# Optimization experiments

Hardware: AMD Instinct MI355X
Metric: run time of the kernel (lower is better)

The kernel has to match this reference:

```python
import jax, jax.numpy as jnp
import numpy as np

OBS, ACT, H, O, B = 256, 64, 1024, 8, 4096
ALPHA, GAMMA, ACT_LIMIT = 0.2, 0.99, 1.0
LOG_STD_MIN, LOG_STD_MAX = -20.0, 2.0
D = OBS + ACT + O  # intra-Q input dim


def setup_inputs() -> dict:
    key = jax.random.key(0)
    ks = iter(jax.random.split(key, 64))
    w = lambda shape: (jax.random.normal(next(ks), shape) * 0.05).astype(jnp.float32)
    inp = {}
    inp["state"] = jax.random.normal(next(ks), (B, OBS), jnp.float32)
    inp["action"] = jnp.tanh(jax.random.normal(next(ks), (B, ACT), jnp.float32))
    inp["next_state"] = jax.random.normal(next(ks), (B, OBS), jnp.float32)
    inp["reward"] = jax.random.normal(next(ks), (B, 1), jnp.float32)
    inp["done"] = jnp.zeros((B, 1), jnp.float32)
    inp["noise"] = jax.random.normal(next(ks), (B, ACT), jnp.float32)
    inp["option"] = jax.random.randint(next(ks), (B,), 0, O, jnp.int32)
    # online inter-Q (q1,q2 stacked on leading axis): obs -> H -> H -> O
    inp["interq_W1"], inp["interq_b1"] = w((2, OBS, H)), w((2, H))
    inp["interq_W2"], inp["interq_b2"] = w((2, H, H)), w((2, H))
    inp["interq_W3"], inp["interq_b3"] = w((2, H, O)), w((2, O))
    # target inter-Q
    inp["tinterq_W1"], inp["tinterq_b1"] = w((2, OBS, H)), w((2, H))
    inp["tinterq_W2"], inp["tinterq_b2"] = w((2, H, H)), w((2, H))
    inp["tinterq_W3"], inp["tinterq_b3"] = w((2, H, O)), w((2, O))
    # intra-Q (q1,q2 stacked): [obs,act,onehot] -> H -> H -> 1
    inp["intraq_W1"], inp["intraq_b1"] = w((2, D, H)), w((2, H))
    inp["intraq_W2"], inp["intraq_b2"] = w((2, H, H)), w((2, H))
    inp["intraq_W3"], inp["intraq_b3"] = w((2, H, 1)), w((2, 1))
    # per-option squashed-Gaussian policies: obs -> H -> H -> (mu, log_std)
    inp["pol_W1"], inp["pol_b1"] = w((O, OBS, H)), w((O, H))
    inp["pol_W2"], inp["pol_b2"] = w((O, H, H)), w((O, H))
    inp["pol_Wmu"], inp["pol_bmu"] = w((O, H, ACT)), w((O, ACT))
    inp["pol_Wls"], inp["pol_bls"] = w((O, H, ACT)), w((O, ACT))
    # per-option termination (beta) nets: obs -> H -> 1, sigmoid
    inp["beta_W1"], inp["beta_b1"] = w((O, OBS, H)), w((O, H))
    inp["beta_W2"], inp["beta_b2"] = w((O, H, 1)), w((O, 1))
    return inp


def _mlp2_k(x, W1, b1, W2, b2, W3, b3):
    # x: [B,in], params stacked over leading k -> [k,B,out]
    h = jax.nn.relu(jnp.einsum('bi,kih->kbh', x, W1) + b1[:, None, :])
    h = jax.nn.relu(jnp.einsum('kbh,khg->kbg', h, W2) + b2[:, None, :])
    return jnp.einsum('kbg,kgo->kbo', h, W3) + b3[:, None, :]


def _forward(state, action, next_state, reward, done, noise,
             interq_W1, interq_b1, interq_W2, interq_b2, interq_W3, interq_b3,
             tinterq_W1, tinterq_b1, tinterq_W2, tinterq_b2, tinterq_W3, tinterq_b3,
             intraq_W1, intraq_b1, intraq_W2, intraq_b2, intraq_W3, intraq_b3,
             pol_W1, pol_b1, pol_W2, pol_b2, pol_Wmu, pol_bmu, pol_Wls, pol_bls,
             beta_W1, beta_b1, beta_W2, beta_b2, option):
    idx = jnp.arange(state.shape[0])
    onehot = jax.nn.one_hot(option, O, dtype=state.dtype)
    # intra Q on (state, action, onehot)
    xq = jnp.concatenate([state, action, onehot], axis=-1)  # [B,D]
    q_intra = _mlp2_k(xq, intraq_W1, intraq_b1, intraq_W2, intraq_b2, intraq_W3, intraq_b3)
    q1_intra, q2_intra = q_intra[0], q_intra[1]  # [B,1]
    # option-routed policy: compute all options, gather top-1 (grouped-MoE form)
    h = jax.nn.relu(jnp.einsum('bi,oih->boh', state, pol_W1) + pol_b1)      # [B,O,H]
    h = jax.nn.relu(jnp.einsum('boh,ohg->bog', h, pol_W2) + pol_b2)         # [B,O,H]
    mu = (jnp.einsum('bog,oga->boa', h, pol_Wmu) + pol_bmu)[idx, option]    # [B,ACT]
    ls = (jnp.einsum('bog,oga->boa', h, pol_Wls) + pol_bls)[idx, option]
    ls = jnp.clip(ls, LOG_STD_MIN, LOG_STD_MAX)
    pre = mu + jnp.exp(ls) * noise  # reparameterized pre-tanh action
    LOG2PI = jnp.float32(np.log(2.0 * np.pi))
    logp = jnp.sum(-0.5 * noise**2 - ls - 0.5 * LOG2PI, axis=-1)
    logp = logp - jnp.sum(2.0 * (jnp.log(jnp.float32(2.0)) - pre - jax.nn.softplus(-2.0 * pre)), axis=-1)  # [B]
    current_actions = ACT_LIMIT * jnp.tanh(pre)  # [B,ACT]
    # option-routed termination prob on next_state
    hb = jax.nn.relu(jnp.einsum('bi,oih->boh', next_state, beta_W1) + beta_b1)
    blog = jnp.einsum('boh,oh->bo', hb, beta_W2[..., 0]) + beta_b2[:, 0]
    beta_prob = jax.nn.sigmoid(blog)[idx, option][:, None]  # [B,1]
    # TD target (no-grad in torch)
    q_t = _mlp2_k(next_state, tinterq_W1, tinterq_b1, tinterq_W2, tinterq_b2, tinterq_W3, tinterq_b3)
    q_inter_targ = jnp.minimum(q_t[0], q_t[1])  # [B,O]
    q_cur = q_inter_targ[idx, option][:, None]
    q_on = _mlp2_k(next_state, interq_W1, interq_b1, interq_W2, interq_b2, interq_W3, interq_b3)
    next_opt = jnp.argmax(jnp.minimum(q_on[0], q_on[1]), axis=-1)  # greedy next option
    q_next = q_inter_targ[idx, next_opt][:, None]
    bp = jax.lax.stop_gradient(beta_prob)
    backup = jax.lax.stop_gradient(
        reward + GAMMA * (1.0 - done) * ((1.0 - bp) * q_cur + bp * q_next))
    loss_intra_q = jnp.mean((q1_intra - backup) ** 2) + jnp.mean((q2_intra - backup) ** 2)
    q_pi = jax.lax.stop_gradient(jnp.minimum(q1_intra, q2_intra))[:, 0]
    loss_intra_pi = jnp.mean(ALPHA * logp - q_pi)
    return (loss_intra_q, loss_intra_pi, current_actions, logp, beta_prob)


def reference(state, action, next_state, reward, done, noise,
              interq_W1, interq_b1, interq_W2, interq_b2, interq_W3, interq_b3,
              tinterq_W1, tinterq_b1, tinterq_W2, tinterq_b2, tinterq_W3, tinterq_b3,
              intraq_W1, intraq_b1, intraq_W2, intraq_b2, intraq_W3, intraq_b3,
              pol_W1, pol_b1, pol_W2, pol_b2, pol_Wmu, pol_bmu, pol_Wls, pol_bls,
              beta_W1, beta_b1, beta_W2, beta_b2, option):
    return _forward(state, action, next_state, reward, done, noise,
                    interq_W1, interq_b1, interq_W2, interq_b2, interq_W3, interq_b3,
                    tinterq_W1, tinterq_b1, tinterq_W2, tinterq_b2, tinterq_W3, tinterq_b3,
                    intraq_W1, intraq_b1, intraq_W2, intraq_b2, intraq_W3, intraq_b3,
                    pol_W1, pol_b1, pol_W2, pol_b2, pol_Wmu, pol_bmu, pol_Wls, pol_bls,
                    beta_W1, beta_b1, beta_W2, beta_b2, option)
```

## Files before the change

kernel.cpp:

```cpp
#include <hip/hip_runtime.h>
#include <stdint.h>

#define B_SZ 4096
#define OBS 256
#define ACT 64
#define HID 1024
#define NOPT 8

typedef __attribute__((ext_vector_type(8))) short short8;
typedef __attribute__((ext_vector_type(4))) float floatx4;
typedef __attribute__((ext_vector_type(4))) unsigned int u32x4;

constexpr long long OFF_WT_I1 = 0;
constexpr long long OFF_WT_I2 = OFF_WT_I1 + 2LL*1024*256*2;
constexpr long long OFF_WT_T1 = OFF_WT_I2 + 2LL*1024*1024*2;
constexpr long long OFF_WT_T2 = OFF_WT_T1 + 2LL*1024*256*2;
constexpr long long OFF_WT_X1 = OFF_WT_T2 + 2LL*1024*1024*2;
constexpr long long OFF_WT_X2 = OFF_WT_X1 + 2LL*1024*384*2;
constexpr long long OFF_WT_P1 = OFF_WT_X2 + 2LL*1024*1024*2;
constexpr long long OFF_WT_P2 = OFF_WT_P1 + 8LL*1024*256*2;
constexpr long long OFF_WT_ML = OFF_WT_P2 + 8LL*1024*1024*2;
constexpr long long OFF_WT_B1 = OFF_WT_ML + 8LL*128*1024*2;
constexpr long long OFF_XQ    = OFF_WT_B1 + 8LL*1024*256*2;
constexpr long long OFF_NS    = OFF_XQ + 4096LL*384*2;
constexpr long long OFF_AGS   = OFF_NS + 4096LL*256*2;
constexpr long long OFF_AGN   = OFF_AGS + 4224LL*256*2;
constexpr long long OFF_HAX   = OFF_AGN + 4224LL*256*2;
constexpr long long OFF_HAI   = OFF_HAX + 2LL*4096*1024*2;
constexpr long long OFF_HAT   = OFF_HAI + 2LL*4096*1024*2;
constexpr long long OFF_HAP   = OFF_HAT + 2LL*4096*1024*2;
constexpr long long OFF_HAB   = OFF_HAP + 4224LL*1024*2;
constexpr long long OFF_HBP   = OFF_HAB + 4224LL*1024*2;
constexpr long long OFF_QI    = OFF_HBP + 4224LL*1024*2;
constexpr long long OFF_QON   = OFF_QI + 2LL*8*4096*4;
constexpr long long OFF_QT    = OFF_QON + 2LL*8*4096*8*4;
constexpr long long OFF_MULS  = OFF_QT + 2LL*8*4096*8*4;
constexpr long long OFF_PERM  = OFF_MULS + 4224LL*128*4;
constexpr long long OFF_OPTG  = OFF_PERM + 4096LL*4;
constexpr long long OFF_BP    = OFF_OPTG + ((4224LL*4 + 255) & ~255LL);
constexpr long long OFF_LOGP  = OFF_BP + 4096LL*4;
constexpr long long OFF_TILEB = OFF_LOGP + 4096LL*4;
constexpr long long OFF_TILEC = OFF_TILEB + 272LL*64;
constexpr long long OFF_TILED = OFF_TILEC + 232LL*64;
constexpr long long WS_TOTAL  = OFF_TILED + 40LL*64;

struct Tile {
  long long aOff, wOff, cOff;
  int mStart, mEnd, K, nCols, flags, biasSel, biasOff, redSel, redOff, pad0;
};
struct Ptrs { const float* bias[9]; const float* w3[3]; };
struct TrSrcs { const float* p[11]; };

__device__ __forceinline__ unsigned short f2bf(float x){
  union { float f; unsigned u; } v; v.f = x;
  unsigned r = v.u + 0x7fffu + ((v.u >> 16) & 1u);
  return (unsigned short)(r >> 16);
}
__device__ __forceinline__ float bf2f(unsigned short h){
  union { float f; unsigned u; } v; v.u = ((unsigned)h) << 16; return v.f;
}

__device__ const long long tr_ws[11] = {256*1024,1024*1024,256*1024,1024*1024,328*1024,1024*1024,256*1024,1024*1024,1024*64,1024*64,256*1024};
__device__ const long long tr_ts[11] = {1024*256,1024*1024,1024*256,1024*1024,1024*384,1024*1024,1024*256,1024*1024,128*1024,128*1024,1024*256};
__device__ const long long tr_dst[11] = {OFF_WT_I1,OFF_WT_I2,OFF_WT_T1,OFF_WT_T2,OFF_WT_X1,OFF_WT_X2,OFF_WT_P1,OFF_WT_P2,OFF_WT_ML,OFF_WT_ML+64LL*1024*2,OFF_WT_B1};

__device__ const int t2_cum[12] = {0,128,640,768,1280,1472,1984,2496,4544,4672,4800,5312};
__device__ const int t2_nk[11]  = {4,16,4,16,6,16,4,16,16,16,4};
__device__ const int t2_N[11]   = {1024,1024,1024,1024,1024,1024,1024,1024,64,64,1024};
__device__ const int t2_K[11]   = {256,1024,256,1024,328,1024,256,1024,1024,1024,256};
__device__ const int t2_Kp[11]  = {256,1024,256,1024,384,1024,256,1024,1024,1024,256};

__global__ __launch_bounds__(256)
void k_tr(char* __restrict__ wsB, TrSrcs srcs){
  __shared__ float lds[64*68];
  int id = blockIdx.x, j = 0;
  while (id >= t2_cum[j+1]) j++;
  int t = id - t2_cum[j];
  int nk = t2_nk[j], nn = t2_N[j] >> 6;
  int per = nk*nn;
  int z = t / per, r = t % per;
  int kt = r % nk, nt = r / nk;
  int K = t2_K[j], Kp = t2_Kp[j], N = t2_N[j];
  const float* src = srcs.p[j] + (long long)z * tr_ws[j];
  unsigned short* dst = (unsigned short*)(wsB + tr_dst[j]) + (long long)z * tr_ts[j];
  int k0 = kt*64, n0 = nt*64;
  int tid = threadIdx.x;
  int kl = tid >> 2, nc = tid & 3;
  int krow = k0 + kl;
  const float* s = src + (long long)krow*N + n0 + nc*16;
  #pragma unroll
  for (int i=0;i<4;i++){
    float4 v = (krow < K) ? *(const float4*)(s + i*4) : make_float4(0.f,0.f,0.f,0.f);
    *(float4*)(&lds[kl*68 + nc*16 + i*4]) = v;
  }
  __syncthreads();
  int nl = tid >> 2, kc = tid & 3;
  unsigned int w[8];
  #pragma unroll
  for (int p=0;p<8;p++){
    float a = lds[(kc*16 + 2*p)*68 + nl];
    float b = lds[(kc*16 + 2*p + 1)*68 + nl];
    w[p] = (unsigned)f2bf(a) | ((unsigned)f2bf(b) << 16);
  }
  u32x4 o0 = {w[0],w[1],w[2],w[3]}, o1 = {w[4],w[5],w[6],w[7]};
  char* d = (char*)(dst + (long long)(n0+nl)*Kp + k0 + kc*16);
  *(u32x4*)d = o0; *(u32x4*)(d + 16) = o1;
}

__global__ void k_route(char* __restrict__ wsB, const int* __restrict__ option,
                        float* __restrict__ out){
  __shared__ int cnt[NOPT], off[NOPT+1], cur[NOPT], ctiles[NOPT], toff[NOPT+1];
  int tid = threadIdx.x;
  int* perm = (int*)(wsB + OFF_PERM);
  int* optg = (int*)(wsB + OFF_OPTG);
  Tile* tb = (Tile*)(wsB + OFF_TILEB);
  Tile* tc = (Tile*)(wsB + OFF_TILEC);
  Tile* tdt = (Tile*)(wsB + OFF_TILED);
  if (tid < NOPT) cnt[tid] = 0;
  __syncthreads();
  for (int b = tid; b < B_SZ; b += 256) atomicAdd(&cnt[option[b]], 1);
  __syncthreads();
  if (tid == 0){
    off[0] = 0; toff[0] = 0;
    for (int o=0;o<NOPT;o++){
      off[o+1] = off[o] + cnt[o];
      ctiles[o] = (cnt[o] + 127) >> 7;
      toff[o+1] = toff[o] + ctiles[o];
      cur[o] = off[o];
    }
    out[0] = 0.f; out[1] = 0.f;
  }
  __syncthreads();
  for (int b = tid; b < B_SZ; b += 256){
    int o = option[b];
    int pos = atomicAdd(&cur[o], 1);
    perm[pos] = b; optg[pos] = o;
  }
  __syncthreads();
  if (tid < 192){
    int task = tid/32, mt = tid%32, z = task&1, net = task>>1;
    int ms = mt*128;
    Tile T{};
    T.mStart = ms; T.mEnd = 4096; T.nCols = 1024; T.flags = 0;
    T.redSel = 0; T.redOff = 0;
    if (net==0){ T.K=384; T.aOff = OFF_XQ + (long long)ms*768; T.wOff = OFF_WT_X1 + (long long)z*786432; T.cOff = OFF_HAX + (long long)z*8388608; T.biasSel=0; }
    else if (net==1){ T.K=256; T.aOff = OFF_NS + (long long)ms*512; T.wOff = OFF_WT_I1 + (long long)z*524288; T.cOff = OFF_HAI + (long long)z*8388608; T.biasSel=1; }
    else { T.K=256; T.aOff = OFF_NS + (long long)ms*512; T.wOff = OFF_WT_T1 + (long long)z*524288; T.cOff = OFF_HAT + (long long)z*8388608; T.biasSel=2; }
    T.biasOff = z*1024;
    tb[tid] = T;
    Tile C{};
    C.mStart = ms; C.mEnd = 4096; C.K = 1024; C.nCols = 1024;
    if (net==0){ C.flags=2; C.aOff = OFF_HAX + (long long)z*8388608 + (long long)ms*2048; C.wOff = OFF_WT_X2 + (long long)z*2097152; C.cOff = OFF_QI + (long long)z*131072; C.biasSel=5; C.redSel=0; C.redOff=z*1024; }
    else if (net==1){ C.flags=3; C.aOff = OFF_HAI + (long long)z*8388608 + (long long)ms*2048; C.wOff = OFF_WT_I2 + (long long)z*2097152; C.cOff = OFF_QON + (long long)z*1048576; C.biasSel=6; C.redSel=1; C.redOff=z*8192; }
    else { C.flags=3; C.aOff = OFF_HAT + (long long)z*8388608 + (long long)ms*2048; C.wOff = OFF_WT_T2 + (long long)z*2097152; C.cOff = OFF_QT + (long long)z*1048576; C.biasSel=7; C.redSel=2; C.redOff=z*8192; }
    C.biasOff = z*1024;
    tc[tid] = C;
  }
  if (tid < NOPT){
    int o = tid, base = toff[o], gs = off[o], ge = off[o+1];
    for (int t=0; t<ctiles[o]; t++){
      int ms = gs + t*128;
      Tile P{};
      P.mStart=ms; P.mEnd=ge; P.K=256; P.nCols=1024; P.flags=0;
      P.aOff = OFF_AGS + (long long)ms*512; P.wOff = OFF_WT_P1 + (long long)o*524288;
      P.cOff = OFF_HAP; P.biasSel=3; P.biasOff=o*1024;
      tb[192 + base + t] = P;
      Tile Bt{};
      Bt.mStart=ms; Bt.mEnd=ge; Bt.K=256; Bt.nCols=1024; Bt.flags=0;
      Bt.aOff = OFF_AGN + (long long)ms*512; Bt.wOff = OFF_WT_B1 + (long long)o*524288;
      Bt.cOff = OFF_HAB; Bt.biasSel=4; Bt.biasOff=o*1024;
      tb[232 + base + t] = Bt;
      Tile C2{};
      C2.mStart=ms; C2.mEnd=ge; C2.K=1024; C2.nCols=1024; C2.flags=0;
      C2.aOff = OFF_HAP + (long long)ms*2048; C2.wOff = OFF_WT_P2 + (long long)o*2097152;
      C2.cOff = OFF_HBP; C2.biasSel=8; C2.biasOff=o*1024;
      tc[192 + base + t] = C2;
      Tile M{};
      M.mStart=ms; M.mEnd=ge; M.K=1024; M.nCols=128; M.flags=1;
      M.aOff = OFF_HBP + (long long)ms*2048; M.wOff = OFF_WT_ML + (long long)o*262144;
      M.cOff = OFF_MULS; M.biasSel=-1;
      tdt[base + t] = M;
    }
  }
  __syncthreads();
  int tT = toff[NOPT];
  for (int s = tT + tid; s < 40; s += 256){
    tb[192+s].K = 0; tb[232+s].K = 0; tc[192+s].K = 0; tdt[s].K = 0;
  }
}

__global__ void k_prep(char* __restrict__ wsB, const float* __restrict__ state,
                       const float* __restrict__ action, const float* __restrict__ nstate,
                       const int* __restrict__ option){
  int blk = blockIdx.x, tid = threadIdx.x;
  const int* perm = (const int*)(wsB + OFF_PERM);
  if (blk < 4224){
    unsigned short* agS = (unsigned short*)(wsB + OFF_AGS);
    unsigned short* agN = (unsigned short*)(wsB + OFF_AGN);
    long long o = (long long)blk*256 + tid;
    if (blk < 4096){
      long long src = (long long)perm[blk]*256 + tid;
      agS[o] = f2bf(state[src]); agN[o] = f2bf(nstate[src]);
    } else { agS[o] = 0; agN[o] = 0; }
  } else if (blk < 8320){
    int b = blk - 4224;
    unsigned short* xq = (unsigned short*)(wsB + OFF_XQ);
    for (int c = tid; c < 384; c += 256){
      float v;
      if (c < 256) v = state[(long long)b*256 + c];
      else if (c < 320) v = action[(long long)b*64 + (c-256)];
      else if (c < 328) v = (option[b] == (c-320)) ? 1.f : 0.f;
      else v = 0.f;
      xq[(long long)b*384 + c] = f2bf(v);
    }
  } else {
    long long i = (long long)(blk-8320)*1024 + tid;
    unsigned short* nsb = (unsigned short*)(wsB + OFF_NS);
    #pragma unroll
    for (int k=0;k<4;k++){ nsb[i] = f2bf(nstate[i]); i += 256; }
  }
}

__global__ __launch_bounds__(256, 2)
void k_gemm(char* __restrict__ wsB, long long tileOff, Ptrs ptrs){
  __shared__ unsigned short As[128*64];
  __shared__ unsigned short Bs[256*64];
  int nx = gridDim.x, T = gridDim.y;
  int id = blockIdx.y*nx + blockIdx.x;
  int xb, yt;
  if ((T & 7) == 0){
    int xcd = id & 7, g = id >> 3;
    xb = g % nx; yt = (g / nx) * 8 + xcd;
  } else { xb = blockIdx.x; yt = blockIdx.y; }
  Tile t = ((const Tile*)(wsB + tileOff))[yt];
  if (t.K == 0) return;
  int n0 = xb * 256;
  if (n0 >= t.nCols) return;

  int tid = threadIdx.x;
  int wave = tid >> 6, lane = tid & 63;
  int wm = wave & 1, wn = wave >> 1;
  int quad = lane >> 4, l16 = lane & 15;

  const floatx4 fzero = {0.f,0.f,0.f,0.f};
  floatx4 acc[4][8];
  #pragma unroll
  for (int mi=0;mi<4;mi++)
    #pragma unroll
    for (int ni=0;ni<8;ni++) acc[mi][ni] = fzero;

  long long rowBytes = (long long)t.K*2;
  const char* Abase = wsB + t.aOff;
  const char* Bbase = wsB + t.wOff + (long long)n0*rowBytes;

  int ra0 = tid >> 2, ka0 = (tid & 3) * 16;
  int ra1 = ra0 + 64;
  const char* gA0 = Abase + (long long)ra0*rowBytes + ka0;
  const char* gA1 = Abase + (long long)ra1*rowBytes + ka0;
  const char* gBp[4];
  #pragma unroll
  for (int j=0;j<4;j++){
    int rb = (tid >> 2) + j*64;
    gBp[j] = Bbase + (long long)rb*rowBytes + ka0;
  }

  u32x4 pA[4], pB[8];
  #define PREFETCH(KBB) { \
    long long _kb = (KBB); \
    pA[0] = *(const u32x4*)(gA0 + _kb);      pA[1] = *(const u32x4*)(gA0 + _kb + 64); \
    pA[2] = *(const u32x4*)(gA1 + _kb);      pA[3] = *(const u32x4*)(gA1 + _kb + 64); \
    _Pragma("unroll") \
    for (int j=0;j<4;j++){ \
      pB[2*j]   = *(const u32x4*)(gBp[j] + _kb); \
      pB[2*j+1] = *(const u32x4*)(gBp[j] + _kb + 64); \
    } }
  #define STAGE() { \
    *(u32x4*)((char*)As + tid*16)         = pA[0]; \
    *(u32x4*)((char*)As + 8192 + tid*16)  = pA[1]; \
    *(u32x4*)((char*)As + 4096 + tid*16)  = pA[2]; \
    *(u32x4*)((char*)As + 12288 + tid*16) = pA[3]; \
    _Pragma("unroll") \
    for (int j=0;j<4;j++){ \
      *(u32x4*)((char*)Bs + j*4096 + tid*16)         = pB[2*j]; \
      *(u32x4*)((char*)Bs + 16384 + j*4096 + tid*16) = pB[2*j+1]; \
    } }

  int nkb = t.K >> 6;
  PREFETCH(0);
  STAGE();
  __syncthreads();
  for (int kb = 0; kb < nkb; kb++){
    if (kb + 1 < nkb) PREFETCH((long long)(kb+1)*128);
    #pragma unroll
    for (int h=0; h<2; h++){
      short8 af[4], bfr[8];
      #pragma unroll
      for (int mi=0;mi<4;mi++)
        af[mi] = *(const short8*)((const char*)As + h*8192 + (wm*64 + mi*16 + l16)*64 + quad*16);
      #pragma unroll
      for (int ni=0;ni<8;ni++)
        bfr[ni] = *(const short8*)((const char*)Bs + h*16384 + (wn*128 + ni*16 + l16)*64 + quad*16);
      #pragma unroll
      for (int mi=0;mi<4;mi++)
        #pragma unroll
        for (int ni=0;ni<8;ni++)
          acc[mi][ni] = __builtin_amdgcn_mfma_f32_16x16x32_bf16(af[mi], bfr[ni], acc[mi][ni], 0, 0, 0);
    }
    __syncthreads();
    if (kb + 1 < nkb){
      STAGE();
      __syncthreads();
    }
  }
  #undef PREFETCH
  #undef STAGE

  if (t.flags <= 1){
    const float* bz = (t.biasSel >= 0) ? (ptrs.bias[t.biasSel] + t.biasOff) : nullptr;
    #pragma unroll
    for (int ni=0;ni<8;ni++){
      int col = n0 + wn*128 + ni*16 + l16;
      if (col >= t.nCols) continue;
      float bval = bz ? bz[col] : 0.f;
      #pragma unroll
      for (int mi=0;mi<4;mi++){
        int rbase = t.mStart + wm*64 + mi*16 + quad*4;
        floatx4 v = acc[mi][ni];
        #pragma unroll
        for (int r=0;r<4;r++){
          int grow = rbase + r;
          if (grow < t.mEnd){
            float x = v[r] + bval;
            if (t.flags == 0){
              x = fmaxf(x, 0.f);
              ((unsigned short*)(wsB + t.cOff))[(long long)grow*t.nCols + col] = f2bf(x);
            } else {
              ((float*)(wsB + t.cOff))[(long long)grow*t.nCols + col] = x;
            }
          }
        }
      }
    }
  } else {
    int NC = (t.flags == 2) ? 1 : 8;
    const float* w3 = ptrs.w3[t.redSel] + t.redOff;
    const float* bz = ptrs.bias[t.biasSel] + t.biasOff;
    int sl = xb*2 + wn;
    float* red = (float*)(wsB + t.cOff) + (long long)sl*4096*NC;
    float bv[8]; int colv[8];
    #pragma unroll
    for (int ni=0;ni<8;ni++){ colv[ni] = n0 + wn*128 + ni*16 + l16; bv[ni] = bz[colv[ni]]; }
    #pragma unroll
    for (int mi=0;mi<4;mi++){
      #pragma unroll
      for (int r=0;r<4;r++){
        int row = t.mStart + wm*64 + mi*16 + quad*4 + r;
        float v[8];
        #pragma unroll
        for (int c=0;c<8;c++) v[c] = 0.f;
        #pragma unroll
        for (int ni=0;ni<8;ni++){
          float x = fmaxf(acc[mi][ni][r] + bv[ni], 0.f);
          if (NC == 1) v[0] += x * w3[colv[ni]];
          else {
            #pragma unroll
            for (int c=0;c<8;c++) v[c] += x * w3[colv[ni]*8 + c];
          }
        }
        for (int c=0;c<NC;c++){
          float s = v[c];
          s += __shfl_xor(s,1); s += __shfl_xor(s,2); s += __shfl_xor(s,4); s += __shfl_xor(s,8);
          if (l16 == 0 && row < t.mEnd) red[(long long)row*NC + c] = s;
        }
      }
    }
  }
}

__global__ void k_bp(char* __restrict__ wsB, const float* __restrict__ noise,
                     const float* __restrict__ bmu, const float* __restrict__ bls,
                     const float* __restrict__ beW2, const float* __restrict__ beb2,
                     float* __restrict__ out){
  int job = blockIdx.x*4 + (threadIdx.x >> 6);
  int lane = threadIdx.x & 63;
  const int* perm = (const int*)(wsB + OFF_PERM);
  const int* optg = (const int*)(wsB + OFF_OPTG);
  if (job < B_SZ){
    int i = job, o = optg[i], b = perm[i];
    const float* muls = (const float*)(wsB + OFF_MULS);
    float* logp = (float*)(wsB + OFF_LOGP);
    float mu = muls[(long long)i*128 + lane] + bmu[o*ACT + lane];
    float ls = muls[(long long)i*128 + 64 + lane] + bls[o*ACT + lane];
    ls = fminf(fmaxf(ls, -20.f), 2.f);
    float nv = noise[(long long)b*ACT + lane];
    float pre = mu + expf(ls)*nv;
    out[2 + (long long)b*ACT + lane] = tanhf(pre);
    float xx = -2.f*pre;
    float sp = fmaxf(xx, 0.f) + log1pf(expf(-fabsf(xx)));
    const float LOG2PI = 1.8378770664093453f;
    const float LN2 = 0.6931471805599453f;
    float lp = -0.5f*nv*nv - ls - 0.5f*LOG2PI - 2.f*(LN2 - pre - sp);
    for (int s=32;s;s>>=1) lp += __shfl_xor(lp, s);
    if (lane == 0){ out[2 + (long long)B_SZ*ACT + b] = lp; logp[b] = lp; }
  } else {
    int i = job - B_SZ, o = optg[i], b = perm[i];
    const char* hrow = wsB + OFF_HAB + (long long)i*2048;
    const float* w = beW2 + (long long)o*HID;
    float* bp = (float*)(wsB + OFF_BP);
    short8 v0 = *(const short8*)(hrow + lane*16);
    short8 v1 = *(const short8*)(hrow + 1024 + lane*16);
    float acc = 0.f;
    #pragma unroll
    for (int e=0;e<8;e++){
      acc += bf2f((unsigned short)v0[e]) * w[lane*8 + e];
      acc += bf2f((unsigned short)v1[e]) * w[512 + lane*8 + e];
    }
    for (int s=32;s;s>>=1) acc += __shfl_xor(acc, s);
    if (lane == 0){
      float v = 1.f/(1.f + expf(-(acc + beb2[o])));
      out[2 + (long long)B_SZ*ACT + B_SZ + b] = v; bp[b] = v;
    }
  }
}

__global__ void k_td(const char* __restrict__ wsB, const int* __restrict__ option,
                     const float* __restrict__ reward, const float* __restrict__ done,
                     const float* __restrict__ xb3, const float* __restrict__ ib3,
                     const float* __restrict__ tb3, float* __restrict__ out){
  int b = blockIdx.x*256 + threadIdx.x;
  const float* qiP  = (const float*)(wsB + OFF_QI);
  const float* qonP = (const float*)(wsB + OFF_QON);
  const float* qtP  = (const float*)(wsB + OFF_QT);
  const float* bp   = (const float*)(wsB + OFF_BP);
  const float* logp = (const float*)(wsB + OFF_LOGP);
  float q1 = xb3[0], q2 = xb3[1];
  #pragma unroll
  for (int sl=0; sl<8; sl++){
    q1 += qiP[sl*4096 + b];
    q2 += qiP[32768 + sl*4096 + b];
  }
  float qons[2][8], qts[2][8];
  #pragma unroll
  for (int z=0;z<2;z++)
    #pragma unroll
    for (int o=0;o<8;o++){ qons[z][o] = ib3[z*8+o]; qts[z][o] = tb3[z*8+o]; }
  for (int z=0;z<2;z++){
    for (int sl=0; sl<8; sl++){
      long long base = ((long long)(z*8 + sl)*4096 + b)*8;
      #pragma unroll
      for (int o=0;o<8;o++){ qons[z][o] += qonP[base+o]; qts[z][o] += qtP[base+o]; }
    }
  }
  float qitv[NOPT];
  #pragma unroll
  for (int o=0;o<NOPT;o++) qitv[o] = fminf(qts[0][o], qts[1][o]);
  float qcur = qitv[option[b]];
  float best = -1e30f; int bo = 0;
  #pragma unroll
  for (int o=0;o<NOPT;o++){
    float v = fminf(qons[0][o], qons[1][o]);
    if (v > best){ best = v; bo = o; }
  }
  float qnext = qitv[bo];
  float bpv = bp[b];
  float backup = reward[b] + 0.99f*(1.f - done[b])*((1.f - bpv)*qcur + bpv*qnext);
  float d1 = q1 - backup, d2 = q2 - backup;
  float tq = d1*d1 + d2*d2;
  float qpi = fminf(q1, q2);
  float tp = 0.2f*logp[b] - qpi;
  for (int s=32;s;s>>=1){ tq += __shfl_xor(tq, s); tp += __shfl_xor(tp, s); }
  __shared__ float sq[4], sp2[4];
  int wave = threadIdx.x>>6, lane = threadIdx.x&63;
  if (lane==0){ sq[wave]=tq; sp2[wave]=tp; }
  __syncthreads();
  if (threadIdx.x==0){
    atomicAdd(&out[0], (sq[0]+sq[1]+sq[2]+sq[3])/(float)B_SZ);
    atomicAdd(&out[1], (sp2[0]+sp2[1]+sp2[2]+sp2[3])/(float)B_SZ);
  }
}

extern "C" void kernel_launch(void* const* d_in, const int* in_sizes, int n_in,
                              void* d_out, int out_size, void* d_ws, size_t ws_size,
                              hipStream_t stream){
  const float* state  = (const float*)d_in[0];
  const float* action = (const float*)d_in[1];
  const float* nstate = (const float*)d_in[2];
  const float* reward = (const float*)d_in[3];
  const float* done   = (const float*)d_in[4];
  const float* noise  = (const float*)d_in[5];
  const int*   option = (const int*)d_in[6];
  const float* iq_W1 = (const float*)d_in[7];  const float* iq_b1 = (const float*)d_in[8];
  const float* iq_W2 = (const float*)d_in[9];  const float* iq_b2 = (const float*)d_in[10];
  const float* iq_W3 = (const float*)d_in[11]; const float* iq_b3 = (const float*)d_in[12];
  const float* tq_W1 = (const float*)d_in[13]; const float* tq_b1 = (const float*)d_in[14];
  const float* tq_W2 = (const float*)d_in[15]; const float* tq_b2 = (const float*)d_in[16];
  const float* tq_W3 = (const float*)d_in[17]; const float* tq_b3 = (const float*)d_in[18];
  const float* xw_W1 = (const float*)d_in[19]; const float* xw_b1 = (const float*)d_in[20];
  const float* xw_W2 = (const float*)d_in[21]; const float* xw_b2 = (const float*)d_in[22];
  const float* xw_W3 = (const float*)d_in[23]; const float* xw_b3 = (const float*)d_in[24];
  const float* p_W1 = (const float*)d_in[25];  const float* p_b1 = (const float*)d_in[26];
  const float* p_W2 = (const float*)d_in[27];  const float* p_b2 = (const float*)d_in[28];
  const float* p_Wmu = (const float*)d_in[29]; const float* p_bmu = (const float*)d_in[30];
  const float* p_Wls = (const float*)d_in[31]; const float* p_bls = (const float*)d_in[32];
  const float* be_W1 = (const float*)d_in[33]; const float* be_b1 = (const float*)d_in[34];
  const float* be_W2 = (const float*)d_in[35]; const float* be_b2 = (const float*)d_in[36];
  float* out = (float*)d_out;
  char* wsB = (char*)d_ws;
  if ((long long)ws_size < WS_TOTAL) return;

  TrSrcs trs;
  trs.p[0]=iq_W1; trs.p[1]=iq_W2; trs.p[2]=tq_W1; trs.p[3]=tq_W2; trs.p[4]=xw_W1;
  trs.p[5]=xw_W2; trs.p[6]=p_W1; trs.p[7]=p_W2; trs.p[8]=p_Wmu; trs.p[9]=p_Wls; trs.p[10]=be_W1;
  Ptrs ptrs;
  ptrs.bias[0]=xw_b1; ptrs.bias[1]=iq_b1; ptrs.bias[2]=tq_b1; ptrs.bias[3]=p_b1; ptrs.bias[4]=be_b1;
  ptrs.bias[5]=xw_b2; ptrs.bias[6]=iq_b2; ptrs.bias[7]=tq_b2; ptrs.bias[8]=p_b2;
  ptrs.w3[0]=xw_W3; ptrs.w3[1]=iq_W3; ptrs.w3[2]=tq_W3;

  k_route<<<1, 256, 0, stream>>>(wsB, option, out);
  k_tr<<<5312, 256, 0, stream>>>(wsB, trs);
  k_prep<<<9344, 256, 0, stream>>>(wsB, state, action, nstate, option);
  k_gemm<<<dim3(4,272), 256, 0, stream>>>(wsB, OFF_TILEB, ptrs);
  k_gemm<<<dim3(4,232), 256, 0, stream>>>(wsB, OFF_TILEC, ptrs);
  k_gemm<<<dim3(1,40), 256, 0, stream>>>(wsB, OFF_TILED, ptrs);
  k_bp<<<2048, 256, 0, stream>>>(wsB, noise, p_bmu, p_bls, be_W2, be_b2, out);
  k_td<<<B_SZ/256, 256, 0, stream>>>(wsB, option, reward, done, xw_b3, iq_b3, tq_b3, out);
}
```

Before: 485.2 us.

## Drop LDS staging in GEMM for direct register loads; split-K the mu/logstd GEMM

The GEMM kernel no longer stages A and B tiles through shared memory. Each wave now loads its MFMA fragments straight from global memory into registers, double-buffered with no barriers. Separately, the small mu/log_std GEMM is split four ways along K into separate partial buffers, which k_bp sums, so the launch grows from 40 to 160 blocks. The aim is to remove LDS traffic and syncs and to raise parallelism in the tail GEMM. In exchange, blocks no longer share tile data, so global and L2 traffic rises and the 16-byte row-strided loads become uncoalesced.

Result: slower. 907.3 us (+87.0%).

```diff
diff --git a/kernel.cpp b/kernel.cpp
--- a/kernel.cpp
+++ b/kernel.cpp
@@ -35,18 +35,19 @@
 constexpr long long OFF_QON   = OFF_QI + 2LL*8*4096*4;
 constexpr long long OFF_QT    = OFF_QON + 2LL*8*4096*8*4;
 constexpr long long OFF_MULS  = OFF_QT + 2LL*8*4096*8*4;
-constexpr long long OFF_PERM  = OFF_MULS + 4224LL*128*4;
+constexpr long long MULS_CH   = 4224LL*128*4;
+constexpr long long OFF_PERM  = OFF_MULS + 4LL*MULS_CH;
 constexpr long long OFF_OPTG  = OFF_PERM + 4096LL*4;
 constexpr long long OFF_BP    = OFF_OPTG + ((4224LL*4 + 255) & ~255LL);
 constexpr long long OFF_LOGP  = OFF_BP + 4096LL*4;
 constexpr long long OFF_TILEB = OFF_LOGP + 4096LL*4;
 constexpr long long OFF_TILEC = OFF_TILEB + 272LL*64;
 constexpr long long OFF_TILED = OFF_TILEC + 232LL*64;
-constexpr long long WS_TOTAL  = OFF_TILED + 40LL*64;
+constexpr long long WS_TOTAL  = OFF_TILED + 160LL*64;
 
 struct Tile {
   long long aOff, wOff, cOff;
-  int mStart, mEnd, K, nCols, flags, biasSel, biasOff, redSel, redOff, pad0;
+  int mStart, mEnd, K, nCols, flags, biasSel, biasOff, redSel, redOff, kLen;
 };
 struct Ptrs { const float* bias[9]; const float* w3[3]; };
 struct TrSrcs { const float* p[11]; };
@@ -146,10 +147,10 @@
     if (net==0){ T.K=384; T.aOff = OFF_XQ + (long long)ms*768; T.wOff = OFF_WT_X1 + (long long)z*786432; T.cOff = OFF_HAX + (long long)z*8388608; T.biasSel=0; }
     else if (net==1){ T.K=256; T.aOff = OFF_NS + (long long)ms*512; T.wOff = OFF_WT_I1 + (long long)z*524288; T.cOff = OFF_HAI + (long long)z*8388608; T.biasSel=1; }
     else { T.K=256; T.aOff = OFF_NS + (long long)ms*512; T.wOff = OFF_WT_T1 + (long long)z*524288; T.cOff = OFF_HAT + (long long)z*8388608; T.biasSel=2; }
-    T.biasOff = z*1024;
+    T.biasOff = z*1024; T.kLen = T.K;
     tb[tid] = T;
     Tile C{};
-    C.mStart = ms; C.mEnd = 4096; C.K = 1024; C.nCols = 1024;
+    C.mStart = ms; C.mEnd = 4096; C.K = 1024; C.nCols = 1024; C.kLen = 1024;
     if (net==0){ C.flags=2; C.aOff = OFF_HAX + (long long)z*8388608 + (long long)ms*2048; C.wOff = OFF_WT_X2 + (long long)z*2097152; C.cOff = OFF_QI + (long long)z*131072; C.biasSel=5; C.redSel=0; C.redOff=z*1024; }
     else if (net==1){ C.flags=3; C.aOff = OFF_HAI + (long long)z*8388608 + (long long)ms*2048; C.wOff = OFF_WT_I2 + (long long)z*2097152; C.cOff = OFF_QON + (long long)z*1048576; C.biasSel=6; C.redSel=1; C.redOff=z*8192; }
     else { C.flags=3; C.aOff = OFF_HAT + (long long)z*8388608 + (long long)ms*2048; C.wOff = OFF_WT_T2 + (long long)z*2097152; C.cOff = OFF_QT + (long long)z*1048576; C.biasSel=7; C.redSel=2; C.redOff=z*8192; }
@@ -161,31 +162,37 @@
     for (int t=0; t<ctiles[o]; t++){
       int ms = gs + t*128;
       Tile P{};
-      P.mStart=ms; P.mEnd=ge; P.K=256; P.nCols=1024; P.flags=0;
+      P.mStart=ms; P.mEnd=ge; P.K=256; P.nCols=1024; P.flags=0; P.kLen=256;
       P.aOff = OFF_AGS + (long long)ms*512; P.wOff = OFF_WT_P1 + (long long)o*524288;
       P.cOff = OFF_HAP; P.biasSel=3; P.biasOff=o*1024;
       tb[192 + base + t] = P;
       Tile Bt{};
-      Bt.mStart=ms; Bt.mEnd=ge; Bt.K=256; Bt.nCols=1024; Bt.flags=0;
+      Bt.mStart=ms; Bt.mEnd=ge; Bt.K=256; Bt.nCols=1024; Bt.flags=0; Bt.kLen=256;
       Bt.aOff = OFF_AGN + (long long)ms*512; Bt.wOff = OFF_WT_B1 + (long long)o*524288;
       Bt.cOff = OFF_HAB; Bt.biasSel=4; Bt.biasOff=o*1024;
       tb[232 + base + t] = Bt;
       Tile C2{};
-      C2.mStart=ms; C2.mEnd=ge; C2.K=1024; C2.nCols=1024; C2.flags=0;
+      C2.mStart=ms; C2.mEnd=ge; C2.K=1024; C2.nCols=1024; C2.flags=0; C2.kLen=1024;
       C2.aOff = OFF_HAP + (long long)ms*2048; C2.wOff = OFF_WT_P2 + (long long)o*2097152;
       C2.cOff = OFF_HBP; C2.biasSel=8; C2.biasOff=o*1024;
       tc[192 + base + t] = C2;
-      Tile M{};
-      M.mStart=ms; M.mEnd=ge; M.K=1024; M.nCols=128; M.flags=1;
-      M.aOff = OFF_HBP + (long long)ms*2048; M.wOff = OFF_WT_ML + (long long)o*262144;
-      M.cOff = OFF_MULS; M.biasSel=-1;
-      tdt[base + t] = M;
+      #pragma unroll
+      for (int c=0;c<4;c++){
+        Tile M{};
+        M.mStart=ms; M.mEnd=ge; M.K=1024; M.nCols=128; M.flags=1; M.kLen=256;
+        M.aOff = OFF_HBP + (long long)ms*2048 + c*512;
+        M.wOff = OFF_WT_ML + (long long)o*262144 + c*512;
+        M.cOff = OFF_MULS + (long long)c*MULS_CH;
+        M.biasSel=-1;
+        tdt[c*40 + base + t] = M;
+      }
     }
   }
   __syncthreads();
   int tT = toff[NOPT];
   for (int s = tT + tid; s < 40; s += 256){
-    tb[192+s].K = 0; tb[232+s].K = 0; tc[192+s].K = 0; tdt[s].K = 0;
+    tb[192+s].kLen = 0; tb[232+s].kLen = 0; tc[192+s].kLen = 0;
+    tdt[s].kLen = 0; tdt[40+s].kLen = 0; tdt[80+s].kLen = 0; tdt[120+s].kLen = 0;
   }
 }
 
@@ -223,8 +230,6 @@
 
 __global__ __launch_bounds__(256, 2)
 void k_gemm(char* __restrict__ wsB, long long tileOff, Ptrs ptrs){
-  __shared__ unsigned short As[128*64];
-  __shared__ unsigned short Bs[256*64];
   int nx = gridDim.x, T = gridDim.y;
   int id = blockIdx.y*nx + blockIdx.x;
   int xb, yt;
@@ -233,7 +238,7 @@
     xb = g % nx; yt = (g / nx) * 8 + xcd;
   } else { xb = blockIdx.x; yt = blockIdx.y; }
   Tile t = ((const Tile*)(wsB + tileOff))[yt];
-  if (t.K == 0) return;
+  if (t.kLen == 0) return;
   int n0 = xb * 256;
   if (n0 >= t.nCols) return;
 
@@ -241,6 +246,7 @@
   int wave = tid >> 6, lane = tid & 63;
   int wm = wave & 1, wn = wave >> 1;
   int quad = lane >> 4, l16 = lane & 15;
+  int n0w = n0 + wn*128;
 
   const floatx4 fzero = {0.f,0.f,0.f,0.f};
   floatx4 acc[4][8];
@@ -249,77 +255,44 @@
     #pragma unroll
     for (int ni=0;ni<8;ni++) acc[mi][ni] = fzero;
 
-  long long rowBytes = (long long)t.K*2;
-  const char* Abase = wsB + t.aOff;
-  const char* Bbase = wsB + t.wOff + (long long)n0*rowBytes;
-
-  int ra0 = tid >> 2, ka0 = (tid & 3) * 16;
-  int ra1 = ra0 + 64;
-  const char* gA0 = Abase + (long long)ra0*rowBytes + ka0;
-  const char* gA1 = Abase + (long long)ra1*rowBytes + ka0;
-  const char* gBp[4];
-  #pragma unroll
-  for (int j=0;j<4;j++){
-    int rb = (tid >> 2) + j*64;
-    gBp[j] = Bbase + (long long)rb*rowBytes + ka0;
-  }
-
-  u32x4 pA[4], pB[8];
-  #define PREFETCH(KBB) { \
-    long long _kb = (KBB); \
-    pA[0] = *(const u32x4*)(gA0 + _kb);      pA[1] = *(const u32x4*)(gA0 + _kb + 64); \
-    pA[2] = *(const u32x4*)(gA1 + _kb);      pA[3] = *(const u32x4*)(gA1 + _kb + 64); \
-    _Pragma("unroll") \
-    for (int j=0;j<4;j++){ \
-      pB[2*j]   = *(const u32x4*)(gBp[j] + _kb); \
-      pB[2*j+1] = *(const u32x4*)(gBp[j] + _kb + 64); \
-    } }
-  #define STAGE() { \
-    *(u32x4*)((char*)As + tid*16)         = pA[0]; \
-    *(u32x4*)((char*)As + 8192 + tid*16)  = pA[1]; \
-    *(u32x4*)((char*)As + 4096 + tid*16)  = pA[2]; \
-    *(u32x4*)((char*)As + 12288 + tid*16) = pA[3]; \
-    _Pragma("unroll") \
-    for (int j=0;j<4;j++){ \
-      *(u32x4*)((char*)Bs + j*4096 + tid*16)         = pB[2*j]; \
-      *(u32x4*)((char*)Bs + 16384 + j*4096 + tid*16) = pB[2*j+1]; \
-    } }
-
-  int nkb = t.K >> 6;
-  PREFETCH(0);
-  STAGE();
-  __syncthreads();
-  for (int kb = 0; kb < nkb; kb++){
-    if (kb + 1 < nkb) PREFETCH((long long)(kb+1)*128);
-    #pragma unroll
-    for (int h=0; h<2; h++){
-      short8 af[4], bfr[8];
-      #pragma unroll
-      for (int mi=0;mi<4;mi++)
-        af[mi] = *(const short8*)((const char*)As + h*8192 + (wm*64 + mi*16 + l16)*64 + quad*16);
-      #pragma unroll
-      for (int ni=0;ni<8;ni++)
-        bfr[ni] = *(const short8*)((const char*)Bs + h*16384 + (wn*128 + ni*16 + l16)*64 + quad*16);
-      #pragma unroll
-      for (int mi=0;mi<4;mi++)
-        #pragma unroll
-        for (int ni=0;ni<8;ni++)
-          acc[mi][ni] = __builtin_amdgcn_mfma_f32_16x16x32_bf16(af[mi], bfr[ni], acc[mi][ni], 0, 0, 0);
-    }
-    __syncthreads();
-    if (kb + 1 < nkb){
-      STAGE();
-      __syncthreads();
-    }
-  }
-  #undef PREFETCH
-  #undef STAGE
+  long long rowB = (long long)t.K*2;
+  const char* Ab = wsB + t.aOff;
+  const char* Bb = wsB + t.wOff;
+  const char* pa[4]; const char* pb[8];
+  #pragma unroll
+  for (int mi=0;mi<4;mi++)
+    pa[mi] = Ab + (long long)(wm*64 + mi*16 + l16)*rowB + quad*16;
+  #pragma unroll
+  for (int ni=0;ni<8;ni++)
+    pb[ni] = Bb + (long long)(n0w + ni*16 + l16)*rowB + quad*16;
+
+  #define LD(dA, dB, KO) { \
+    _Pragma("unroll") for (int mi=0;mi<4;mi++) dA[mi] = *(const short8*)(pa[mi] + (KO)); \
+    _Pragma("unroll") for (int ni=0;ni<8;ni++) dB[ni] = *(const short8*)(pb[ni] + (KO)); }
+  #define MM(sA, sB) { \
+    _Pragma("unroll") for (int mi=0;mi<4;mi++) \
+      _Pragma("unroll") for (int ni=0;ni<8;ni++) \
+        acc[mi][ni] = __builtin_amdgcn_mfma_f32_16x16x32_bf16(sA[mi], sB[ni], acc[mi][ni], 0, 0, 0); }
+
+  int nkb = t.kLen >> 5;
+  short8 aC[4], bC[8], aN[4], bN[8];
+  LD(aC, bC, 0);
+  LD(aN, bN, 64);
+  for (int kb = 0; kb < nkb; kb += 2){
+    long long ko = (long long)kb*64;
+    MM(aC, bC);
+    if (kb + 2 < nkb) LD(aC, bC, ko + 128);
+    MM(aN, bN);
+    if (kb + 3 < nkb) LD(aN, bN, ko + 192);
+  }
+  #undef LD
+  #undef MM
 
   if (t.flags <= 1){
     const float* bz = (t.biasSel >= 0) ? (ptrs.bias[t.biasSel] + t.biasOff) : nullptr;
     #pragma unroll
     for (int ni=0;ni<8;ni++){
-      int col = n0 + wn*128 + ni*16 + l16;
+      int col = n0w + ni*16 + l16;
       if (col >= t.nCols) continue;
       float bval = bz ? bz[col] : 0.f;
       #pragma unroll
@@ -349,7 +322,7 @@
     float* red = (float*)(wsB + t.cOff) + (long long)sl*4096*NC;
     float bv[8]; int colv[8];
     #pragma unroll
-    for (int ni=0;ni<8;ni++){ colv[ni] = n0 + wn*128 + ni*16 + l16; bv[ni] = bz[colv[ni]]; }
+    for (int ni=0;ni<8;ni++){ colv[ni] = n0w + ni*16 + l16; bv[ni] = bz[colv[ni]]; }
     #pragma unroll
     for (int mi=0;mi<4;mi++){
       #pragma unroll
@@ -389,8 +362,13 @@
     int i = job, o = optg[i], b = perm[i];
     const float* muls = (const float*)(wsB + OFF_MULS);
     float* logp = (float*)(wsB + OFF_LOGP);
-    float mu = muls[(long long)i*128 + lane] + bmu[o*ACT + lane];
-    float ls = muls[(long long)i*128 + 64 + lane] + bls[o*ACT + lane];
+    float mu = bmu[o*ACT + lane];
+    float ls = bls[o*ACT + lane];
+    #pragma unroll
+    for (int c=0;c<4;c++){
+      mu += muls[(long long)c*(MULS_CH/4) + (long long)i*128 + lane];
+      ls += muls[(long long)c*(MULS_CH/4) + (long long)i*128 + 64 + lane];
+    }
     ls = fminf(fmaxf(ls, -20.f), 2.f);
     float nv = noise[(long long)b*ACT + lane];
     float pre = mu + expf(ls)*nv;
@@ -521,7 +499,7 @@
   k_prep<<<9344, 256, 0, stream>>>(wsB, state, action, nstate, option);
   k_gemm<<<dim3(4,272), 256, 0, stream>>>(wsB, OFF_TILEB, ptrs);
   k_gemm<<<dim3(4,232), 256, 0, stream>>>(wsB, OFF_TILEC, ptrs);
-  k_gemm<<<dim3(1,40), 256, 0, stream>>>(wsB, OFF_TILED, ptrs);
+  k_gemm<<<dim3(1,160), 256, 0, stream>>>(wsB, OFF_TILED, ptrs);
   k_bp<<<2048, 256, 0, stream>>>(wsB, noise, p_bmu, p_bls, be_W2, be_b2, out);
   k_td<<<B_SZ/256, 256, 0, stream>>>(wsB, option, reward, done, xw_b3, iq_b3, tq_b3, out);
 }
```

## Split policy head GEMM along K into four chunks, merge transpose into prep

Applied to the files above, without the earlier changes.

The mu/log-std head GEMM (K=1024, only 128 columns, 40 tiles) is split into four K-chunks of 256. Each chunk writes its own partial buffer, and k_bp sums the four partials, so the launch has 160 blocks instead of 40 and keeps more of the GPU busy. The weight-transpose kernel is folded into k_prep as extra blocks, which removes one launch and lets the two jobs overlap. The gemm kernel is also split into three identically compiled kernels. In exchange, the head needs more workspace and k_bp does extra partial-sum reads.

Measured after the change: 468.1 us. 1.04x faster.

```diff
diff --git a/kernel.cpp b/kernel.cpp
--- a/kernel.cpp
+++ b/kernel.cpp
@@ -35,18 +35,19 @@
 constexpr long long OFF_QON   = OFF_QI + 2LL*8*4096*4;
 constexpr long long OFF_QT    = OFF_QON + 2LL*8*4096*8*4;
 constexpr long long OFF_MULS  = OFF_QT + 2LL*8*4096*8*4;
-constexpr long long OFF_PERM  = OFF_MULS + 4224LL*128*4;
+constexpr long long MULS_CH   = 4224LL*128*4;
+constexpr long long OFF_PERM  = OFF_MULS + 4LL*MULS_CH;
 constexpr long long OFF_OPTG  = OFF_PERM + 4096LL*4;
 constexpr long long OFF_BP    = OFF_OPTG + ((4224LL*4 + 255) & ~255LL);
 constexpr long long OFF_LOGP  = OFF_BP + 4096LL*4;
 constexpr long long OFF_TILEB = OFF_LOGP + 4096LL*4;
 constexpr long long OFF_TILEC = OFF_TILEB + 272LL*64;
 constexpr long long OFF_TILED = OFF_TILEC + 232LL*64;
-constexpr long long WS_TOTAL  = OFF_TILED + 40LL*64;
+constexpr long long WS_TOTAL  = OFF_TILED + 160LL*64;
 
 struct Tile {
   long long aOff, wOff, cOff;
-  int mStart, mEnd, K, nCols, flags, biasSel, biasOff, redSel, redOff, pad0;
+  int mStart, mEnd, K, nCols, flags, biasSel, biasOff, redSel, redOff, kLen;
 };
 struct Ptrs { const float* bias[9]; const float* w3[3]; };
 struct TrSrcs { const float* p[11]; };
@@ -63,49 +64,11 @@
 __device__ const long long tr_ws[11] = {256*1024,1024*1024,256*1024,1024*1024,328*1024,1024*1024,256*1024,1024*1024,1024*64,1024*64,256*1024};
 __device__ const long long tr_ts[11] = {1024*256,1024*1024,1024*256,1024*1024,1024*384,1024*1024,1024*256,1024*1024,128*1024,128*1024,1024*256};
 __device__ const long long tr_dst[11] = {OFF_WT_I1,OFF_WT_I2,OFF_WT_T1,OFF_WT_T2,OFF_WT_X1,OFF_WT_X2,OFF_WT_P1,OFF_WT_P2,OFF_WT_ML,OFF_WT_ML+64LL*1024*2,OFF_WT_B1};
-
 __device__ const int t2_cum[12] = {0,128,640,768,1280,1472,1984,2496,4544,4672,4800,5312};
 __device__ const int t2_nk[11]  = {4,16,4,16,6,16,4,16,16,16,4};
 __device__ const int t2_N[11]   = {1024,1024,1024,1024,1024,1024,1024,1024,64,64,1024};
 __device__ const int t2_K[11]   = {256,1024,256,1024,328,1024,256,1024,1024,1024,256};
 __device__ const int t2_Kp[11]  = {256,1024,256,1024,384,1024,256,1024,1024,1024,256};
-
-__global__ __launch_bounds__(256)
-void k_tr(char* __restrict__ wsB, TrSrcs srcs){
-  __shared__ float lds[64*68];
-  int id = blockIdx.x, j = 0;
-  while (id >= t2_cum[j+1]) j++;
-  int t = id - t2_cum[j];
-  int nk = t2_nk[j], nn = t2_N[j] >> 6;
-  int per = nk*nn;
-  int z = t / per, r = t % per;
-  int kt = r % nk, nt = r / nk;
-  int K = t2_K[j], Kp = t2_Kp[j], N = t2_N[j];
-  const float* src = srcs.p[j] + (long long)z * tr_ws[j];
-  unsigned short* dst = (unsigned short*)(wsB + tr_dst[j]) + (long long)z * tr_ts[j];
-  int k0 = kt*64, n0 = nt*64;
-  int tid = threadIdx.x;
-  int kl = tid >> 2, nc = tid & 3;
-  int krow = k0 + kl;
-  const float* s = src + (long long)krow*N + n0 + nc*16;
-  #pragma unroll
-  for (int i=0;i<4;i++){
-    float4 v = (krow < K) ? *(const float4*)(s + i*4) : make_float4(0.f,0.f,0.f,0.f);
-    *(float4*)(&lds[kl*68 + nc*16 + i*4]) = v;
-  }
-  __syncthreads();
-  int nl = tid >> 2, kc = tid & 3;
-  unsigned int w[8];
-  #pragma unroll
-  for (int p=0;p<8;p++){
-    float a = lds[(kc*16 + 2*p)*68 + nl];
-    float b = lds[(kc*16 + 2*p + 1)*68 + nl];
-    w[p] = (unsigned)f2bf(a) | ((unsigned)f2bf(b) << 16);
-  }
-  u32x4 o0 = {w[0],w[1],w[2],w[3]}, o1 = {w[4],w[5],w[6],w[7]};
-  char* d = (char*)(dst + (long long)(n0+nl)*Kp + k0 + kc*16);
-  *(u32x4*)d = o0; *(u32x4*)(d + 16) = o1;
-}
 
 __global__ void k_route(char* __restrict__ wsB, const int* __restrict__ option,
                         float* __restrict__ out){
@@ -146,10 +109,10 @@
     if (net==0){ T.K=384; T.aOff = OFF_XQ + (long long)ms*768; T.wOff = OFF_WT_X1 + (long long)z*786432; T.cOff = OFF_HAX + (long long)z*8388608; T.biasSel=0; }
     else if (net==1){ T.K=256; T.aOff = OFF_NS + (long long)ms*512; T.wOff = OFF_WT_I1 + (long long)z*524288; T.cOff = OFF_HAI + (long long)z*8388608; T.biasSel=1; }
     else { T.K=256; T.aOff = OFF_NS + (long long)ms*512; T.wOff = OFF_WT_T1 + (long long)z*524288; T.cOff = OFF_HAT + (long long)z*8388608; T.biasSel=2; }
-    T.biasOff = z*1024;
+    T.biasOff = z*1024; T.kLen = T.K;
     tb[tid] = T;
     Tile C{};
-    C.mStart = ms; C.mEnd = 4096; C.K = 1024; C.nCols = 1024;
+    C.mStart = ms; C.mEnd = 4096; C.K = 1024; C.nCols = 1024; C.kLen = 1024;
     if (net==0){ C.flags=2; C.aOff = OFF_HAX + (long long)z*8388608 + (long long)ms*2048; C.wOff = OFF_WT_X2 + (long long)z*2097152; C.cOff = OFF_QI + (long long)z*131072; C.biasSel=5; C.redSel=0; C.redOff=z*1024; }
     else if (net==1){ C.flags=3; C.aOff = OFF_HAI + (long long)z*8388608 + (long long)ms*2048; C.wOff = OFF_WT_I2 + (long long)z*2097152; C.cOff = OFF_QON + (long long)z*1048576; C.biasSel=6; C.redSel=1; C.redOff=z*8192; }
     else { C.flags=3; C.aOff = OFF_HAT + (long long)z*8388608 + (long long)ms*2048; C.wOff = OFF_WT_T2 + (long long)z*2097152; C.cOff = OFF_QT + (long long)z*1048576; C.biasSel=7; C.redSel=2; C.redOff=z*8192; }
@@ -161,38 +124,81 @@
     for (int t=0; t<ctiles[o]; t++){
       int ms = gs + t*128;
       Tile P{};
-      P.mStart=ms; P.mEnd=ge; P.K=256; P.nCols=1024; P.flags=0;
+      P.mStart=ms; P.mEnd=ge; P.K=256; P.nCols=1024; P.flags=0; P.kLen=256;
       P.aOff = OFF_AGS + (long long)ms*512; P.wOff = OFF_WT_P1 + (long long)o*524288;
       P.cOff = OFF_HAP; P.biasSel=3; P.biasOff=o*1024;
       tb[192 + base + t] = P;
       Tile Bt{};
-      Bt.mStart=ms; Bt.mEnd=ge; Bt.K=256; Bt.nCols=1024; Bt.flags=0;
+      Bt.mStart=ms; Bt.mEnd=ge; Bt.K=256; Bt.nCols=1024; Bt.flags=0; Bt.kLen=256;
       Bt.aOff = OFF_AGN + (long long)ms*512; Bt.wOff = OFF_WT_B1 + (long long)o*524288;
       Bt.cOff = OFF_HAB; Bt.biasSel=4; Bt.biasOff=o*1024;
       tb[232 + base + t] = Bt;
       Tile C2{};
-      C2.mStart=ms; C2.mEnd=ge; C2.K=1024; C2.nCols=1024; C2.flags=0;
+      C2.mStart=ms; C2.mEnd=ge; C2.K=1024; C2.nCols=1024; C2.flags=0; C2.kLen=1024;
       C2.aOff = OFF_HAP + (long long)ms*2048; C2.wOff = OFF_WT_P2 + (long long)o*2097152;
       C2.cOff = OFF_HBP; C2.biasSel=8; C2.biasOff=o*1024;
       tc[192 + base + t] = C2;
-      Tile M{};
-      M.mStart=ms; M.mEnd=ge; M.K=1024; M.nCols=128; M.flags=1;
-      M.aOff = OFF_HBP + (long long)ms*2048; M.wOff = OFF_WT_ML + (long long)o*262144;
-      M.cOff = OFF_MULS; M.biasSel=-1;
-      tdt[base + t] = M;
+      #pragma unroll
+      for (int c=0;c<4;c++){
+        Tile M{};
+        M.mStart=ms; M.mEnd=ge; M.K=1024; M.nCols=128; M.flags=1; M.kLen=256;
+        M.aOff = OFF_HBP + (long long)ms*2048 + c*512;
+        M.wOff = OFF_WT_ML + (long long)o*262144 + c*512;
+        M.cOff = OFF_MULS + (long long)c*MULS_CH;
+        M.biasSel=-1;
+        tdt[c*40 + base + t] = M;
+      }
     }
   }
   __syncthreads();
   int tT = toff[NOPT];
   for (int s = tT + tid; s < 40; s += 256){
-    tb[192+s].K = 0; tb[232+s].K = 0; tc[192+s].K = 0; tdt[s].K = 0;
-  }
-}
-
-__global__ void k_prep(char* __restrict__ wsB, const float* __restrict__ state,
-                       const float* __restrict__ action, const float* __restrict__ nstate,
-                       const int* __restrict__ option){
-  int blk = blockIdx.x, tid = threadIdx.x;
+    tb[192+s].kLen = 0; tb[232+s].kLen = 0; tc[192+s].kLen = 0;
+    tdt[s].kLen = 0; tdt[40+s].kLen = 0; tdt[80+s].kLen = 0; tdt[120+s].kLen = 0;
+  }
+}
+
+__global__ __launch_bounds__(256)
+void k_prep(char* __restrict__ wsB, TrSrcs srcs, const float* __restrict__ state,
+            const float* __restrict__ action, const float* __restrict__ nstate,
+            const int* __restrict__ option){
+  __shared__ float lds[64*68];
+  int blk0 = blockIdx.x, tid = threadIdx.x;
+  if (blk0 < 5312){
+    int id = blk0, j = 0;
+    while (id >= t2_cum[j+1]) j++;
+    int t = id - t2_cum[j];
+    int nk = t2_nk[j], nn = t2_N[j] >> 6;
+    int per = nk*nn;
+    int z = t / per, r = t % per;
+    int kt = r % nk, nt = r / nk;
+    int K = t2_K[j], Kp = t2_Kp[j], N = t2_N[j];
+    const float* src = srcs.p[j] + (long long)z * tr_ws[j];
+    unsigned short* dst = (unsigned short*)(wsB + tr_dst[j]) + (long long)z * tr_ts[j];
+    int k0 = kt*64, n0 = nt*64;
+    int kl = tid >> 2, nc = tid & 3;
+    int krow = k0 + kl;
+    const float* s = src + (long long)krow*N + n0 + nc*16;
+    #pragma unroll
+    for (int i=0;i<4;i++){
+      float4 v = (krow < K) ? *(const float4*)(s + i*4) : make_float4(0.f,0.f,0.f,0.f);
+      *(float4*)(&lds[kl*68 + nc*16 + i*4]) = v;
+    }
+    __syncthreads();
+    int nl = tid >> 2, kc = tid & 3;
+    unsigned int w[8];
+    #pragma unroll
+    for (int p=0;p<8;p++){
+      float a = lds[(kc*16 + 2*p)*68 + nl];
+      float b = lds[(kc*16 + 2*p + 1)*68 + nl];
+      w[p] = (unsigned)f2bf(a) | ((unsigned)f2bf(b) << 16);
+    }
+    u32x4 o0 = {w[0],w[1],w[2],w[3]}, o1 = {w[4],w[5],w[6],w[7]};
+    char* d = (char*)(dst + (long long)(n0+nl)*Kp + k0 + kc*16);
+    *(u32x4*)d = o0; *(u32x4*)(d + 16) = o1;
+    return;
+  }
+  int blk = blk0 - 5312;
   const int* perm = (const int*)(wsB + OFF_PERM);
   if (blk < 4224){
     unsigned short* agS = (unsigned short*)(wsB + OFF_AGS);
@@ -221,8 +227,7 @@
   }
 }
 
-__global__ __launch_bounds__(256, 2)
-void k_gemm(char* __restrict__ wsB, long long tileOff, Ptrs ptrs){
+__device__ __forceinline__ void gemm_body(char* __restrict__ wsB, long long tileOff, const Ptrs& ptrs){
   __shared__ unsigned short As[128*64];
   __shared__ unsigned short Bs[256*64];
   int nx = gridDim.x, T = gridDim.y;
@@ -233,7 +238,7 @@
     xb = g % nx; yt = (g / nx) * 8 + xcd;
   } else { xb = blockIdx.x; yt = blockIdx.y; }
   Tile t = ((const Tile*)(wsB + tileOff))[yt];
-  if (t.K == 0) return;
+  if (t.kLen == 0) return;
   int n0 = xb * 256;
   if (n0 >= t.nCols) return;
 
@@ -285,7 +290,7 @@
       *(u32x4*)((char*)Bs + 16384 + j*4096 + tid*16) = pB[2*j+1]; \
     } }
 
-  int nkb = t.K >> 6;
+  int nkb = t.kLen >> 6;
   PREFETCH(0);
   STAGE();
   __syncthreads();
@@ -377,6 +382,13 @@
   }
 }
 
+__global__ __launch_bounds__(256, 2)
+void k_gemm_l1(char* __restrict__ wsB, long long tileOff, Ptrs ptrs){ gemm_body(wsB, tileOff, ptrs); }
+__global__ __launch_bounds__(256, 2)
+void k_gemm_l2(char* __restrict__ wsB, long long tileOff, Ptrs ptrs){ gemm_body(wsB, tileOff, ptrs); }
+__global__ __launch_bounds__(256, 2)
+void k_gemm_hd(char* __restrict__ wsB, long long tileOff, Ptrs ptrs){ gemm_body(wsB, tileOff, ptrs); }
+
 __global__ void k_bp(char* __restrict__ wsB, const float* __restrict__ noise,
                      const float* __restrict__ bmu, const float* __restrict__ bls,
                      const float* __restrict__ beW2, const float* __restrict__ beb2,
@@ -389,8 +401,13 @@
     int i = job, o = optg[i], b = perm[i];
     const float* muls = (const float*)(wsB + OFF_MULS);
     float* logp = (float*)(wsB + OFF_LOGP);
-    float mu = muls[(long long)i*128 + lane] + bmu[o*ACT + lane];
-    float ls = muls[(long long)i*128 + 64 + lane] + bls[o*ACT + lane];
+    float mu = bmu[o*ACT + lane];
+    float ls = bls[o*ACT + lane];
+    #pragma unroll
+    for (int c=0;c<4;c++){
+      mu += muls[(long long)c*(MULS_CH/4) + (long long)i*128 + lane];
+      ls += muls[(long long)c*(MULS_CH/4) + (long long)i*128 + 64 + lane];
+    }
     ls = fminf(fmaxf(ls, -20.f), 2.f);
     float nv = noise[(long long)b*ACT + lane];
     float pre = mu + expf(ls)*nv;
@@ -517,11 +534,10 @@
   ptrs.w3[0]=xw_W3; ptrs.w3[1]=iq_W3; ptrs.w3[2]=tq_W3;
 
   k_route<<<1, 256, 0, stream>>>(wsB, option, out);
-  k_tr<<<5312, 256, 0, stream>>>(wsB, trs);
-  k_prep<<<9344, 256, 0, stream>>>(wsB, state, action, nstate, option);
-  k_gemm<<<dim3(4,272), 256, 0, stream>>>(wsB, OFF_TILEB, ptrs);
-  k_gemm<<<dim3(4,232), 256, 0, stream>>>(wsB, OFF_TILEC, ptrs);
-  k_gemm<<<dim3(1,40), 256, 0, stream>>>(wsB, OFF_TILED, ptrs);
+  k_prep<<<5312 + 9344, 256, 0, stream>>>(wsB, trs, state, action, nstate, option);
+  k_gemm_l1<<<dim3(4,272), 256, 0, stream>>>(wsB, OFF_TILEB, ptrs);
+  k_gemm_l2<<<dim3(4,232), 256, 0, stream>>>(wsB, OFF_TILEC, ptrs);
+  k_gemm_hd<<<dim3(1,160), 256, 0, stream>>>(wsB, OFF_TILED, ptrs);
   k_bp<<<2048, 256, 0, stream>>>(wsB, noise, p_bmu, p_bls, be_W2, be_b2, out);
   k_td<<<B_SZ/256, 256, 0, stream>>>(wsB, option, reward, done, xw_b3, iq_b3, tq_b3, out);
 }
```
